# Kernel tuning notes

Hardware: AMD Instinct MI355X
Metric: run time of the kernel (lower is better)

## Reference

```python
import jax, jax.numpy as jnp
import numpy as np

N_NODES = 100000
N_EDGES = 1600000
D_FEAT = 128
N_CLASSES = 10


def setup_inputs() -> dict:
    key = jax.random.key(0)
    ks = jax.random.split(key, 9)
    x = jax.random.normal(ks[0], (N_NODES, D_FEAT), dtype=jnp.float32)
    edge_src = jax.random.randint(ks[1], (N_EDGES,), 0, N_NODES, dtype=jnp.int32)
    edge_dst = jax.random.randint(ks[2], (N_EDGES,), 0, N_NODES, dtype=jnp.int32)
    s = 1.0 / np.sqrt(D_FEAT)
    W1 = jax.random.normal(ks[3], (D_FEAT, D_FEAT), dtype=jnp.float32) * s
    b1 = jax.random.normal(ks[4], (D_FEAT,), dtype=jnp.float32) * s
    W2 = jax.random.normal(ks[5], (D_FEAT, D_FEAT), dtype=jnp.float32) * s
    b2 = jax.random.normal(ks[6], (D_FEAT,), dtype=jnp.float32) * s
    W3 = jax.random.normal(ks[7], (D_FEAT, N_CLASSES), dtype=jnp.float32) * s
    b3 = jax.random.normal(ks[8], (N_CLASSES,), dtype=jnp.float32) * s
    return {"x": x, "edge_src": edge_src, "edge_dst": edge_dst,
            "W1": W1, "b1": b1, "W2": W2, "b2": b2, "W3": W3, "b3": b3}


def _neighbor_mean(x, src, dst, n_nodes):
    # scatter-mean of neighbor features; isolated nodes keep their own feature
    msg_sum = jax.ops.segment_sum(x[src], dst, num_segments=n_nodes)  # [N, D]
    deg = jax.ops.segment_sum(jnp.ones(src.shape, x.dtype), dst, num_segments=n_nodes)  # [N]
    mean = msg_sum / jnp.maximum(deg, 1.0)[:, None]
    return jnp.where(deg[:, None] > 0, mean, x)


def reference(x, edge_src, edge_dst, W1, b1, W2, b2, W3, b3):
    n = x.shape[0]
    # layer 1: aggregate -> linear -> tanh
    h = jnp.tanh(_neighbor_mean(x, edge_src, edge_dst, n) @ W1 + b1)
    # layer 2: aggregate -> linear -> tanh
    h = jnp.tanh(_neighbor_mean(h, edge_src, edge_dst, n) @ W2 + b2)
    # final linear head (no aggregation, no activation)
    logits = h @ W3 + b3
    return logits
```

## Files before the change

### kernel.cpp

```cpp
#include <hip/hip_runtime.h>

#define DF 128
#define AST 136
#define EPB 2048

typedef float f32x4 __attribute__((ext_vector_type(4)));
typedef short bf16x8 __attribute__((ext_vector_type(8)));

__device__ __forceinline__ ushort f2bf(float f) {
  union { float f; uint u; } c; c.f = f;
  uint u = c.u;
  uint r = (u + 0x7fffu + ((u >> 16) & 1u)) >> 16;
  return (ushort)r;
}
__device__ __forceinline__ float bf_lo(uint v) { union { uint u; float f; } c; c.u = v << 16; return c.f; }
__device__ __forceinline__ float bf_hi(uint v) { union { uint u; float f; } c; c.u = v & 0xffff0000u; return c.f; }

__device__ __forceinline__ void addv8(float* acc, uint4 v) {
  acc[0] += bf_lo(v.x); acc[1] += bf_hi(v.x);
  acc[2] += bf_lo(v.y); acc[3] += bf_hi(v.y);
  acc[4] += bf_lo(v.z); acc[5] += bf_hi(v.z);
  acc[6] += bf_lo(v.w); acc[7] += bf_hi(v.w);
}

__global__ void prep_kernel(const float* __restrict__ x, ushort* __restrict__ xb,
                            const float* __restrict__ W1, ushort* __restrict__ Wt1,
                            const float* __restrict__ W2, ushort* __restrict__ Wt2,
                            const float* __restrict__ W3, ushort* __restrict__ W3t,
                            ushort* __restrict__ xbN, ushort* __restrict__ bufBN, int n4) {
  int i = blockIdx.x * 256 + threadIdx.x;
  if (i < n4) {
    float4 v = ((const float4*)x)[i];
    ushort4 o; o.x = f2bf(v.x); o.y = f2bf(v.y); o.z = f2bf(v.z); o.w = f2bf(v.w);
    ((ushort4*)xb)[i] = o;
    return;
  }
  int j = i - n4;
  if (j < DF * DF) {
    int nr = j >> 7, k = j & 127;
    Wt1[j] = f2bf(W1[(size_t)k * DF + nr]);
    return;
  }
  j -= DF * DF;
  if (j < DF * DF) {
    int nr = j >> 7, k = j & 127;
    Wt2[j] = f2bf(W2[(size_t)k * DF + nr]);
    return;
  }
  j -= DF * DF;
  if (j < 16 * DF) {
    int nr = j >> 7, k = j & 127;
    W3t[j] = (nr < 10) ? f2bf(W3[(size_t)k * 10 + nr]) : (ushort)0;
    return;
  }
  j -= 16 * DF;
  if (j < 16) { ((uint4*)xbN)[j] = (uint4){0, 0, 0, 0}; return; }
  j -= 16;
  if (j < 16) { ((uint4*)bufBN)[j] = (uint4){0, 0, 0, 0}; }
}


__global__ void bucket_hist_kernel(const int* __restrict__ dst, int* __restrict__ histG,
                                   int E, int nbuck, int nblocks) {
  extern __shared__ int lh[];
  int tid = threadIdx.x, blk = blockIdx.x;
  for (int i = tid; i < nbuck; i += 256) lh[i] = 0;
  __syncthreads();
  int base = blk * EPB;
#pragma unroll
  for (int it = 0; it < EPB / 256; ++it) {
    int e = base + it * 256 + tid;
    if (e < E) atomicAdd(&lh[dst[e] >> 8], 1);
  }
  __syncthreads();
  for (int i = tid; i < nbuck; i += 256) histG[(size_t)i * nblocks + blk] = lh[i];
}

__global__ void scan1_kernel(const int* __restrict__ cnt, int* __restrict__ excl,
                             int* __restrict__ bsums, int n) {
  __shared__ int wsum[4];
  int t = threadIdx.x;
  int base = blockIdx.x * 1024 + t * 4;
  int v[4]; int s = 0;
#pragma unroll
  for (int i = 0; i < 4; i++) { int d = (base + i < n) ? cnt[base + i] : 0; v[i] = s; s += d; }
  int lane = t & 63, w = t >> 6;
  int sc = s;
#pragma unroll
  for (int off = 1; off < 64; off <<= 1) { int o = __shfl_up(sc, off); if (lane >= off) sc += o; }
  if (lane == 63) wsum[w] = sc;
  __syncthreads();
  int woff = 0;
  for (int i = 0; i < w; i++) woff += wsum[i];
  int toff = woff + (sc - s);
#pragma unroll
  for (int i = 0; i < 4; i++) if (base + i < n) excl[base + i] = toff + v[i];
  if (t == 255) bsums[blockIdx.x] = woff + sc;
}

__global__ void scan2_kernel(int* bsums, int nb) {
  __shared__ int wsum[16];
  int t = threadIdx.x;
  int v = (t < nb) ? bsums[t] : 0;
  int lane = t & 63, w = t >> 6;
  int sc = v;
#pragma unroll
  for (int off = 1; off < 64; off <<= 1) { int o = __shfl_up(sc, off); if (lane >= off) sc += o; }
  if (lane == 63) wsum[w] = sc;
  __syncthreads();
  int woff = 0;
  for (int i = 0; i < w; i++) woff += wsum[i];
  if (t < nb) bsums[t] = woff + sc - v;
}

__global__ void bucket_scatter_kernel(const int* __restrict__ src, const int* __restrict__ dst,
                                      const int* __restrict__ histE, const int* __restrict__ bsums,
                                      uint* __restrict__ eb, int E, int nbuck, int nblocks) {
  extern __shared__ int lc[];
  int tid = threadIdx.x, blk = blockIdx.x;
  for (int i = tid; i < nbuck; i += 256) {
    int idx = i * nblocks + blk;
    lc[i] = histE[idx] + bsums[idx >> 10];
  }
  __syncthreads();
  int base = blk * EPB;
#pragma unroll
  for (int it = 0; it < EPB / 256; ++it) {
    int e = base + it * 256 + tid;
    if (e < E) {
      int d = dst[e];
      int pos = atomicAdd(&lc[d >> 8], 1);
      eb[pos] = (uint)src[e] | ((uint)(d & 255) << 24);
    }
  }
}

__global__ void bucket_sort_kernel(const uint* __restrict__ eb,
                                   const int* __restrict__ histE, const int* __restrict__ bsums,
                                   int* __restrict__ rowptr, int* __restrict__ csr,
                                   int N, int E, int nbuck, int nblocks) {
  __shared__ int cnt[256];
  __shared__ int cursor[256];
  __shared__ int wsum[4];
  int tid = threadIdx.x, b = blockIdx.x;
  int idx = b * nblocks;
  int beg = histE[idx] + bsums[idx >> 10];
  int end = E;
  if (b + 1 < nbuck) { int i2 = (b + 1) * nblocks; end = histE[i2] + bsums[i2 >> 10]; }
  cnt[tid] = 0;
  __syncthreads();
  for (int e = beg + tid; e < end; e += 256)
    atomicAdd(&cnt[eb[e] >> 24], 1);
  __syncthreads();
  int v = cnt[tid];
  int lane = tid & 63, w = tid >> 6;
  int sc = v;
#pragma unroll
  for (int off = 1; off < 64; off <<= 1) { int o = __shfl_up(sc, off); if (lane >= off) sc += o; }
  if (lane == 63) wsum[w] = sc;
  __syncthreads();
  int woff = 0;
  for (int i = 0; i < w; i++) woff += wsum[i];
  int excl = woff + sc - v;
  int node = (b << 8) + tid;
  if (node <= N) rowptr[node] = beg + excl;
  cursor[tid] = beg + excl;
  __syncthreads();
  for (int e = beg + tid; e < end; e += 256) {
    uint vv = eb[e];
    int pos = atomicAdd(&cursor[vv >> 24], 1);
    csr[pos] = (int)(vv & 0x00FFFFFFu);
  }
}

__global__ __launch_bounds__(256) void aggregate_kernel(
    const ushort* __restrict__ xb, const int* __restrict__ rowptr,
    const int* __restrict__ csr, ushort* __restrict__ out, int n) {
  int gw = (blockIdx.x * 256 + threadIdx.x) >> 6;
  int lane = threadIdx.x & 63;
  if (gw >= n) return;
  int beg = rowptr[gw], end = rowptr[gw + 1];
  int g = lane >> 4;
  uint coff = (uint)(lane & 15) * 16u;
  const char* xbase = (const char*)xb;
  float acc[8];
#pragma unroll
  for (int i = 0; i < 8; i++) acc[i] = 0.f;

#pragma unroll 1
  for (int e = beg; e < end; e += 16) {
    int e0 = e + g, e1 = e + 4 + g, e2 = e + 8 + g, e3 = e + 12 + g;
    int last = end - 1;
    int i0 = csr[e0 < end ? e0 : last];
    int i1 = csr[e1 < end ? e1 : last];
    int i2 = csr[e2 < end ? e2 : last];
    int i3 = csr[e3 < end ? e3 : last];
    uint r0 = (e0 < end) ? (uint)i0 : (uint)n;
    uint r1 = (e1 < end) ? (uint)i1 : (uint)n;
    uint r2 = (e2 < end) ? (uint)i2 : (uint)n;
    uint r3 = (e3 < end) ? (uint)i3 : (uint)n;
    uint4 v0 = *(const uint4*)(xbase + (r0 * 256u + coff));
    uint4 v1 = *(const uint4*)(xbase + (r1 * 256u + coff));
    uint4 v2 = *(const uint4*)(xbase + (r2 * 256u + coff));
    uint4 v3 = *(const uint4*)(xbase + (r3 * 256u + coff));
    addv8(acc, v0);
    addv8(acc, v1);
    addv8(acc, v2);
    addv8(acc, v3);
  }

#pragma unroll
  for (int i = 0; i < 8; i++) {
    acc[i] += __shfl_xor(acc[i], 16);
    acc[i] += __shfl_xor(acc[i], 32);
  }

  int deg = end - beg;
  if (lane < 16) {
    uint4 r;
    if (deg > 0) {
      float inv = 1.0f / (float)deg;
      r.x = (uint)f2bf(acc[0] * inv) | ((uint)f2bf(acc[1] * inv) << 16);
      r.y = (uint)f2bf(acc[2] * inv) | ((uint)f2bf(acc[3] * inv) << 16);
      r.z = (uint)f2bf(acc[4] * inv) | ((uint)f2bf(acc[5] * inv) << 16);
      r.w = (uint)f2bf(acc[6] * inv) | ((uint)f2bf(acc[7] * inv) << 16);
    } else {
      r = *(const uint4*)(xbase + ((uint)gw * 256u + coff));
    }
    *(uint4*)((char*)out + ((uint)gw * 256u + coff)) = r;
  }
}

__global__ __launch_bounds__(256) void gemm_tanh_mfma(
    const ushort* __restrict__ A, const ushort* __restrict__ Wt,
    const float* __restrict__ bias, ushort* __restrict__ out, int n) {
  __shared__ ushort As[64 * AST];
  __shared__ ushort Ws[128 * AST];
  int tid = threadIdx.x;
  int node0 = blockIdx.x * 64;

  for (int i = tid; i < 64 * 16; i += 256) {
    int r = i >> 4, c = i & 15;
    int node = node0 + r; if (node >= n) node = n - 1;
    uint4 v = ((const uint4*)(A + (size_t)node * DF))[c];
    *(uint4*)&As[r * AST + c * 8] = v;
  }
  for (int i = tid; i < 128 * 16; i += 256) {
    int r = i >> 4, c = i & 15;
    uint4 v = ((const uint4*)(Wt + r * DF))[c];
    *(uint4*)&Ws[r * AST + c * 8] = v;
  }
  __syncthreads();

  int lane = tid & 63, w = tid >> 6;
  int wr = (w >> 1) * 32;
  int wc = (w & 1) * 64;
  int r16 = lane & 15, g8 = (lane >> 4) * 8;

  f32x4 acc[2][4];
#pragma unroll
  for (int i = 0; i < 2; i++)
#pragma unroll
    for (int j = 0; j < 4; j++) acc[i][j] = (f32x4){0.f, 0.f, 0.f, 0.f};

#pragma unroll
  for (int ks = 0; ks < 4; ++ks) {
    int k0 = ks * 32 + g8;
    bf16x8 a0 = *(const bf16x8*)&As[(wr + r16) * AST + k0];
    bf16x8 a1 = *(const bf16x8*)&As[(wr + 16 + r16) * AST + k0];
#pragma unroll
    for (int j = 0; j < 4; j++) {
      bf16x8 b = *(const bf16x8*)&Ws[(wc + j * 16 + r16) * AST + k0];
      acc[0][j] = __builtin_amdgcn_mfma_f32_16x16x32_bf16(a0, b, acc[0][j], 0, 0, 0);
      acc[1][j] = __builtin_amdgcn_mfma_f32_16x16x32_bf16(a1, b, acc[1][j], 0, 0, 0);
    }
  }

#pragma unroll
  for (int mi = 0; mi < 2; mi++) {
#pragma unroll
    for (int j = 0; j < 4; j++) {
      int col = wc + j * 16 + r16;
      float bv = bias[col];
      int rowb = wr + mi * 16 + (lane >> 4) * 4;
#pragma unroll
      for (int q = 0; q < 4; q++) {
        int node = node0 + rowb + q;
        if (node < n) {
          float vv = tanhf(acc[mi][j][q] + bv);
          out[(size_t)node * DF + col] = f2bf(vv);
        }
      }
    }
  }
}

__global__ __launch_bounds__(256) void gemm2_head_mfma(
    const ushort* __restrict__ A, const ushort* __restrict__ Wt,
    const float* __restrict__ bias, const ushort* __restrict__ W3t,
    const float* __restrict__ b3, float* __restrict__ out, int n) {
  __shared__ ushort As[64 * AST];
  __shared__ ushort Ws[128 * AST];
  __shared__ ushort W3s[16 * AST];
  int tid = threadIdx.x;
  int node0 = blockIdx.x * 64;

  for (int i = tid; i < 64 * 16; i += 256) {
    int r = i >> 4, c = i & 15;
    int node = node0 + r; if (node >= n) node = n - 1;
    uint4 v = ((const uint4*)(A + (size_t)node * DF))[c];
    *(uint4*)&As[r * AST + c * 8] = v;
  }
  for (int i = tid; i < 128 * 16; i += 256) {
    int r = i >> 4, c = i & 15;
    uint4 v = ((const uint4*)(Wt + r * DF))[c];
    *(uint4*)&Ws[r * AST + c * 8] = v;
  }
  {
    int r = tid >> 4, c = tid & 15;
    uint4 v = ((const uint4*)(W3t + r * DF))[c];
    *(uint4*)&W3s[r * AST + c * 8] = v;
  }
  __syncthreads();

  int lane = tid & 63, w = tid >> 6;
  int wr = (w >> 1) * 32, wc = (w & 1) * 64;
  int r16 = lane & 15, g8 = (lane >> 4) * 8;

  f32x4 acc[2][4];
#pragma unroll
  for (int i = 0; i < 2; i++)
#pragma unroll
    for (int j = 0; j < 4; j++) acc[i][j] = (f32x4){0.f, 0.f, 0.f, 0.f};

#pragma unroll
  for (int ks = 0; ks < 4; ++ks) {
    int k0 = ks * 32 + g8;
    bf16x8 a0 = *(const bf16x8*)&As[(wr + r16) * AST + k0];
    bf16x8 a1 = *(const bf16x8*)&As[(wr + 16 + r16) * AST + k0];
#pragma unroll
    for (int j = 0; j < 4; ++j) {
      bf16x8 b = *(const bf16x8*)&Ws[(wc + j * 16 + r16) * AST + k0];
      acc[0][j] = __builtin_amdgcn_mfma_f32_16x16x32_bf16(a0, b, acc[0][j], 0, 0, 0);
      acc[1][j] = __builtin_amdgcn_mfma_f32_16x16x32_bf16(a1, b, acc[1][j], 0, 0, 0);
    }
  }

  __syncthreads();
#pragma unroll
  for (int mi = 0; mi < 2; mi++) {
#pragma unroll
    for (int j = 0; j < 4; j++) {
      int col = wc + j * 16 + r16;
      float bv = bias[col];
      int rowb = wr + mi * 16 + (lane >> 4) * 4;
#pragma unroll
      for (int q = 0; q < 4; q++)
        As[(rowb + q) * AST + col] = f2bf(tanhf(acc[mi][j][q] + bv));
    }
  }
  __syncthreads();

  f32x4 h = (f32x4){0.f, 0.f, 0.f, 0.f};
#pragma unroll
  for (int ks = 0; ks < 4; ++ks) {
    int k0 = ks * 32 + g8;
    bf16x8 a = *(const bf16x8*)&As[(w * 16 + r16) * AST + k0];
    bf16x8 b = *(const bf16x8*)&W3s[r16 * AST + k0];
    h = __builtin_amdgcn_mfma_f32_16x16x32_bf16(a, b, h, 0, 0, 0);
  }
  if (r16 < 10) {
    float bv = b3[r16];
    int rowb = w * 16 + (lane >> 4) * 4;
#pragma unroll
    for (int q = 0; q < 4; q++) {
      int node = node0 + rowb + q;
      if (node < n) out[(size_t)node * 10 + r16] = h[q] + bv;
    }
  }
}

extern "C" void kernel_launch(void* const* d_in, const int* in_sizes, int n_in,
                              void* d_out, int out_size, void* d_ws, size_t ws_size,
                              hipStream_t stream) {
  const float* x    = (const float*)d_in[0];
  const int*   esrc = (const int*)d_in[1];
  const int*   edst = (const int*)d_in[2];
  const float* W1   = (const float*)d_in[3];
  const float* b1   = (const float*)d_in[4];
  const float* W2   = (const float*)d_in[5];
  const float* b2   = (const float*)d_in[6];
  const float* W3   = (const float*)d_in[7];
  const float* b3   = (const float*)d_in[8];
  float* out = (float*)d_out;

  const int N = in_sizes[0] / DF;
  const int E = in_sizes[1];

  const int nbuck   = (N + 255) >> 8;
  const int nblocks = (E + EPB - 1) / EPB;
  const int M = nbuck * nblocks;

  char* ws = (char*)d_ws;
  int*  rowptr = (int*)ws;
  int*  csr    = rowptr + (N + 1);
  int*  histG  = csr + E;
  int*  histE  = histG + M;
  int*  bsums2 = histE + M;
  uint* eb     = (uint*)(bsums2 + 1024);
  size_t off = (size_t)((char*)(eb + E) - ws);
  off = (off + 255) & ~(size_t)255;
  ushort* xb  = (ushort*)(ws + off);     off += (size_t)(N + 1) * DF * 2; off = (off + 255) & ~(size_t)255;
  ushort* Wt1 = (ushort*)(ws + off);     off += (size_t)DF * DF * 2;
  ushort* Wt2 = (ushort*)(ws + off);     off += (size_t)DF * DF * 2;
  ushort* W3t = (ushort*)(ws + off);     off += (size_t)16 * DF * 2; off = (off + 255) & ~(size_t)255;
  ushort* bufA = (ushort*)(ws + off);    off += (size_t)N * DF * 2; off = (off + 255) & ~(size_t)255;
  ushort* bufB = (ushort*)(ws + off);

  int n4 = N * DF / 4;
  int prep_total = n4 + 2 * DF * DF + 16 * DF + 32;
  prep_kernel<<<(prep_total + 255) / 256, 256, 0, stream>>>(
      x, xb, W1, Wt1, W2, Wt2, W3, W3t, xb + (size_t)N * DF, bufB + (size_t)N * DF, n4);

  size_t lds_b = (size_t)nbuck * sizeof(int);
  bucket_hist_kernel<<<nblocks, 256, lds_b, stream>>>(edst, histG, E, nbuck, nblocks);
  int nb_m = (M + 1023) / 1024;
  scan1_kernel<<<nb_m, 256, 0, stream>>>(histG, histE, bsums2, M);
  scan2_kernel<<<1, 1024, 0, stream>>>(bsums2, nb_m);
  bucket_scatter_kernel<<<nblocks, 256, lds_b, stream>>>(esrc, edst, histE, bsums2, eb, E, nbuck, nblocks);
  bucket_sort_kernel<<<nbuck, 256, 0, stream>>>(eb, histE, bsums2, rowptr, csr, N, E, nbuck, nblocks);

  int agg_blocks = (N * 64 + 255) / 256;
  int gemm_blocks = (N + 63) / 64;

  aggregate_kernel<<<agg_blocks, 256, 0, stream>>>(xb, rowptr, csr, bufA, N);
  gemm_tanh_mfma<<<gemm_blocks, 256, 0, stream>>>(bufA, Wt1, b1, bufB, N);
  aggregate_kernel<<<agg_blocks, 256, 0, stream>>>(bufB, rowptr, csr, bufA, N);
  gemm2_head_mfma<<<gemm_blocks, 256, 0, stream>>>(bufA, Wt2, b2, W3t, b3, out, N);
}
```

Measured before the change: 226.1 us.

## Aggregate one node per 16 lanes and read GEMM weights from global

The aggregation kernel now gives each node 16 lanes instead of a full 64-lane wavefront. Each thread walks that node's edges serially four at a time, so the cross-lane shuffle reduction and the idle lanes on low-degree nodes go away. Separately, both GEMM kernels stop staging the weight matrices in LDS and load B fragments directly from global memory, relying on the cache. This cuts LDS use and the per-block weight copy, which should raise occupancy, but it puts repeated global/L2 weight reads in the MFMA inner loop.

```diff
diff --git a/kernel.cpp b/kernel.cpp
--- a/kernel.cpp
+++ b/kernel.cpp
@@ -176,66 +176,52 @@
 __global__ __launch_bounds__(256) void aggregate_kernel(
     const ushort* __restrict__ xb, const int* __restrict__ rowptr,
     const int* __restrict__ csr, ushort* __restrict__ out, int n) {
-  int gw = (blockIdx.x * 256 + threadIdx.x) >> 6;
-  int lane = threadIdx.x & 63;
-  if (gw >= n) return;
-  int beg = rowptr[gw], end = rowptr[gw + 1];
-  int g = lane >> 4;
-  uint coff = (uint)(lane & 15) * 16u;
+  int tid = threadIdx.x;
+  int node = (blockIdx.x * 256 + tid) >> 4;
+  if (node >= n) return;
+  uint c16 = (uint)(tid & 15) * 16u;
+  int beg = rowptr[node], end = rowptr[node + 1];
   const char* xbase = (const char*)xb;
   float acc[8];
 #pragma unroll
   for (int i = 0; i < 8; i++) acc[i] = 0.f;
 
 #pragma unroll 1
-  for (int e = beg; e < end; e += 16) {
-    int e0 = e + g, e1 = e + 4 + g, e2 = e + 8 + g, e3 = e + 12 + g;
+  for (int e = beg; e < end; e += 4) {
     int last = end - 1;
-    int i0 = csr[e0 < end ? e0 : last];
-    int i1 = csr[e1 < end ? e1 : last];
-    int i2 = csr[e2 < end ? e2 : last];
-    int i3 = csr[e3 < end ? e3 : last];
-    uint r0 = (e0 < end) ? (uint)i0 : (uint)n;
-    uint r1 = (e1 < end) ? (uint)i1 : (uint)n;
-    uint r2 = (e2 < end) ? (uint)i2 : (uint)n;
-    uint r3 = (e3 < end) ? (uint)i3 : (uint)n;
-    uint4 v0 = *(const uint4*)(xbase + (r0 * 256u + coff));
-    uint4 v1 = *(const uint4*)(xbase + (r1 * 256u + coff));
-    uint4 v2 = *(const uint4*)(xbase + (r2 * 256u + coff));
-    uint4 v3 = *(const uint4*)(xbase + (r3 * 256u + coff));
+    int e1 = e + 1, e2 = e + 2, e3 = e + 3;
+    uint r0 = (uint)csr[e];
+    uint r1 = (e1 < end) ? (uint)csr[e1] : (uint)n;
+    uint r2 = (e2 < end) ? (uint)csr[e2] : (uint)n;
+    uint r3 = (e3 < end) ? (uint)csr[e3] : (uint)n;
+    uint4 v0 = *(const uint4*)(xbase + (r0 * 256u + c16));
+    uint4 v1 = *(const uint4*)(xbase + (r1 * 256u + c16));
+    uint4 v2 = *(const uint4*)(xbase + (r2 * 256u + c16));
+    uint4 v3 = *(const uint4*)(xbase + (r3 * 256u + c16));
     addv8(acc, v0);
     addv8(acc, v1);
     addv8(acc, v2);
     addv8(acc, v3);
   }
 
-#pragma unroll
-  for (int i = 0; i < 8; i++) {
-    acc[i] += __shfl_xor(acc[i], 16);
-    acc[i] += __shfl_xor(acc[i], 32);
-  }
-
   int deg = end - beg;
-  if (lane < 16) {
-    uint4 r;
-    if (deg > 0) {
-      float inv = 1.0f / (float)deg;
-      r.x = (uint)f2bf(acc[0] * inv) | ((uint)f2bf(acc[1] * inv) << 16);
-      r.y = (uint)f2bf(acc[2] * inv) | ((uint)f2bf(acc[3] * inv) << 16);
-      r.z = (uint)f2bf(acc[4] * inv) | ((uint)f2bf(acc[5] * inv) << 16);
-      r.w = (uint)f2bf(acc[6] * inv) | ((uint)f2bf(acc[7] * inv) << 16);
-    } else {
-      r = *(const uint4*)(xbase + ((uint)gw * 256u + coff));
-    }
-    *(uint4*)((char*)out + ((uint)gw * 256u + coff)) = r;
-  }
+  uint4 r;
+  if (deg > 0) {
+    float inv = 1.0f / (float)deg;
+    r.x = (uint)f2bf(acc[0] * inv) | ((uint)f2bf(acc[1] * inv) << 16);
+    r.y = (uint)f2bf(acc[2] * inv) | ((uint)f2bf(acc[3] * inv) << 16);
+    r.z = (uint)f2bf(acc[4] * inv) | ((uint)f2bf(acc[5] * inv) << 16);
+    r.w = (uint)f2bf(acc[6] * inv) | ((uint)f2bf(acc[7] * inv) << 16);
+  } else {
+    r = *(const uint4*)(xbase + ((uint)node * 256u + c16));
+  }
+  *(uint4*)((char*)out + ((uint)node * 256u + c16)) = r;
 }
 
 __global__ __launch_bounds__(256) void gemm_tanh_mfma(
     const ushort* __restrict__ A, const ushort* __restrict__ Wt,
     const float* __restrict__ bias, ushort* __restrict__ out, int n) {
   __shared__ ushort As[64 * AST];
-  __shared__ ushort Ws[128 * AST];
   int tid = threadIdx.x;
   int node0 = blockIdx.x * 64;
 
@@ -245,11 +231,6 @@
     uint4 v = ((const uint4*)(A + (size_t)node * DF))[c];
     *(uint4*)&As[r * AST + c * 8] = v;
   }
-  for (int i = tid; i < 128 * 16; i += 256) {
-    int r = i >> 4, c = i & 15;
-    uint4 v = ((const uint4*)(Wt + r * DF))[c];
-    *(uint4*)&Ws[r * AST + c * 8] = v;
-  }
   __syncthreads();
 
   int lane = tid & 63, w = tid >> 6;
@@ -270,7 +251,7 @@
     bf16x8 a1 = *(const bf16x8*)&As[(wr + 16 + r16) * AST + k0];
 #pragma unroll
     for (int j = 0; j < 4; j++) {
-      bf16x8 b = *(const bf16x8*)&Ws[(wc + j * 16 + r16) * AST + k0];
+      bf16x8 b = *(const bf16x8*)&Wt[(wc + j * 16 + r16) * DF + k0];
       acc[0][j] = __builtin_amdgcn_mfma_f32_16x16x32_bf16(a0, b, acc[0][j], 0, 0, 0);
       acc[1][j] = __builtin_amdgcn_mfma_f32_16x16x32_bf16(a1, b, acc[1][j], 0, 0, 0);
     }
@@ -300,8 +281,6 @@
     const float* __restrict__ bias, const ushort* __restrict__ W3t,
     const float* __restrict__ b3, float* __restrict__ out, int n) {
   __shared__ ushort As[64 * AST];
-  __shared__ ushort Ws[128 * AST];
-  __shared__ ushort W3s[16 * AST];
   int tid = threadIdx.x;
   int node0 = blockIdx.x * 64;
 
@@ -311,16 +290,6 @@
     uint4 v = ((const uint4*)(A + (size_t)node * DF))[c];
     *(uint4*)&As[r * AST + c * 8] = v;
   }
-  for (int i = tid; i < 128 * 16; i += 256) {
-    int r = i >> 4, c = i & 15;
-    uint4 v = ((const uint4*)(Wt + r * DF))[c];
-    *(uint4*)&Ws[r * AST + c * 8] = v;
-  }
-  {
-    int r = tid >> 4, c = tid & 15;
-    uint4 v = ((const uint4*)(W3t + r * DF))[c];
-    *(uint4*)&W3s[r * AST + c * 8] = v;
-  }
   __syncthreads();
 
   int lane = tid & 63, w = tid >> 6;
@@ -340,7 +309,7 @@
     bf16x8 a1 = *(const bf16x8*)&As[(wr + 16 + r16) * AST + k0];
 #pragma unroll
     for (int j = 0; j < 4; ++j) {
-      bf16x8 b = *(const bf16x8*)&Ws[(wc + j * 16 + r16) * AST + k0];
+      bf16x8 b = *(const bf16x8*)&Wt[(wc + j * 16 + r16) * DF + k0];
       acc[0][j] = __builtin_amdgcn_mfma_f32_16x16x32_bf16(a0, b, acc[0][j], 0, 0, 0);
       acc[1][j] = __builtin_amdgcn_mfma_f32_16x16x32_bf16(a1, b, acc[1][j], 0, 0, 0);
     }
@@ -366,7 +335,7 @@
   for (int ks = 0; ks < 4; ++ks) {
     int k0 = ks * 32 + g8;
     bf16x8 a = *(const bf16x8*)&As[(w * 16 + r16) * AST + k0];
-    bf16x8 b = *(const bf16x8*)&W3s[r16 * AST + k0];
+    bf16x8 b = *(const bf16x8*)&W3t[r16 * DF + k0];
     h = __builtin_amdgcn_mfma_f32_16x16x32_bf16(a, b, h, 0, 0, 0);
   }
   if (r16 < 10) {
@@ -430,7 +399,7 @@
   bucket_scatter_kernel<<<nblocks, 256, lds_b, stream>>>(esrc, edst, histE, bsums2, eb, E, nbuck, nblocks);
   bucket_sort_kernel<<<nbuck, 256, 0, stream>>>(eb, histE, bsums2, rowptr, csr, N, E, nbuck, nblocks);
 
-  int agg_blocks = (N * 64 + 255) / 256;
+  int agg_blocks = (N + 15) / 16;
   int gemm_blocks = (N + 63) / 64;
 
   aggregate_kernel<<<agg_blocks, 256, 0, stream>>>(xb, rowptr, csr, bufA, N);
```

Result: slower. 234.7 us (+3.8%).
